# Performance work log

Measured on AMD Instinct MI355X. Metric: run time of the kernel, lower is better.

Reference implementation:

```python
import jax, jax.numpy as jnp
import numpy as np

N_NODES = 100000


def _gcn_conv(h, src, dst, W, b, n_nodes):
    """PyG GCNConv with add_self_loops=True, symmetric normalization.
    out = D^-1/2 (A + I) D^-1/2 (h W) + b, aggregating src->dst."""
    h = h @ W  # transform first (out_dim <= in_dim), as PyG does
    ones = jnp.ones(src.shape[0], dtype=h.dtype)
    deg = jax.ops.segment_sum(ones, dst, num_segments=n_nodes) + 1.0  # +1 self loop
    dinv = jax.lax.rsqrt(deg)
    coef = dinv[src] * dinv[dst]  # per-edge norm
    agg = jax.ops.segment_sum(h[src] * coef[:, None], dst, num_segments=n_nodes)
    agg = agg + h * (dinv * dinv)[:, None]  # self-loop term: dinv_i^2 * h_i
    return agg + b


def setup_inputs() -> dict:
    key = jax.random.key(0)
    k1, k2, k3, k4 = jax.random.split(key, 4)
    x = jax.random.normal(k1, (N_NODES, 256), dtype=jnp.float32)
    edge_index = jax.random.randint(k2, (2, 1600000), 0, N_NODES, dtype=jnp.int64)
    W1 = jax.random.normal(k3, (256, 128), dtype=jnp.float32) * (1.0 / np.sqrt(256))
    b1 = jnp.zeros((128,), dtype=jnp.float32)
    W2 = jax.random.normal(k4, (128, 64), dtype=jnp.float32) * (1.0 / np.sqrt(128))
    b2 = jnp.zeros((64,), dtype=jnp.float32)
    return {"x": x, "edge_index": edge_index, "W1": W1, "b1": b1, "W2": W2, "b2": b2}


def reference(x, edge_index, W1, b1, W2, b2):
    src, dst = edge_index[0], edge_index[1]
    h = jax.nn.relu(_gcn_conv(x, src, dst, W1, b1, N_NODES))
    # dropout is identity in eval mode
    h = _gcn_conv(h, src, dst, W2, b2, N_NODES)
    return jax.nn.log_softmax(h, axis=1)
```

## Files before the change

### kernel.cpp

```cpp
#include <hip/hip_runtime.h>
#include <hip/hip_bf16.h>


#define N_NODES 100000
#define F_IN 256
#define F_MID 128
#define F_OUT 64

#define BSHIFT 8
#define BNODES 256
#define NBUCKETS ((N_NODES + BNODES - 1) / BNODES)
#define BCAP 6144
#define EPB 4096

typedef __attribute__((ext_vector_type(8))) short short8;
typedef __attribute__((ext_vector_type(4))) float f32x4;

__device__ inline ushort bf16_rne(float f) {
    uint u = __float_as_uint(f);
    u += 0x7FFF + ((u >> 16) & 1);
    return (ushort)(u >> 16);
}
__device__ inline float lo16(uint r) { return __uint_as_float(r << 16); }
__device__ inline float hi16(uint r) { return __uint_as_float(r & 0xffff0000u); }
__device__ inline uint pack_bf2(float a, float b) {
    return (uint)bf16_rne(a) | ((uint)bf16_rne(b) << 16);
}


__global__ __launch_bounds__(256)
void bucket_scatter_kernel(const int* __restrict__ src, const int* __restrict__ dst,
                           int* __restrict__ bcur, uint* __restrict__ ebuf, int E) {
    __shared__ int curL[NBUCKETS];
    int t = threadIdx.x;
    int e0 = blockIdx.x * EPB;
    int e1 = e0 + EPB; if (e1 > E) e1 = E;

    for (int i = t; i < NBUCKETS; i += 256) curL[i] = 0;
    __syncthreads();
    for (int i = e0 + t; i < e1; i += 256) atomicAdd(&curL[dst[i] >> BSHIFT], 1);
    __syncthreads();
    for (int i = t; i < NBUCKETS; i += 256) {
        int h = curL[i];
        curL[i] = h ? atomicAdd(&bcur[i], h) : 0;
    }
    __syncthreads();
    for (int i = e0 + t; i < e1; i += 256) {
        int d = dst[i], s = src[i];
        int b = d >> BSHIFT;
        int pos = atomicAdd(&curL[b], 1);
        if (pos < BCAP) ebuf[(size_t)b * BCAP + pos] = ((uint)(d & (BNODES - 1)) << 17) | (uint)s;
    }
}

__global__ __launch_bounds__(256)
void bucket_sort_kernel(const uint* __restrict__ ebuf, const int* __restrict__ bcur,
                        int* __restrict__ ssrc, int* __restrict__ rs, int* __restrict__ cnt,
                        float* __restrict__ dinv, int n) {
    __shared__ uint eL[BCAP];
    __shared__ int hist[BNODES], ps[BNODES];
    int b = blockIdx.x, t = threadIdx.x;
    int nb = bcur[b];
    if (nb > BCAP) nb = BCAP;
    for (int i = t; i < nb; i += 256) eL[i] = ebuf[(size_t)b * BCAP + i];
    hist[t] = 0;
    __syncthreads();
    for (int i = t; i < nb; i += 256) atomicAdd(&hist[eL[i] >> 17], 1);
    __syncthreads();
    ps[t] = hist[t];
    __syncthreads();
#pragma unroll
    for (int off = 1; off < BNODES; off <<= 1) {
        int v = (t >= off) ? ps[t - off] : 0;
        __syncthreads();
        ps[t] += v;
        __syncthreads();
    }
    int excl = ps[t] - hist[t];
    int node = b * BNODES + t;
    if (node < n) {
        rs[node] = b * BCAP + excl;
        cnt[node] = hist[t];
        dinv[node] = 1.0f / sqrtf((float)hist[t] + 1.0f);
    }
    __syncthreads();
    ps[t] = excl;
    __syncthreads();
    for (int i = t; i < nb; i += 256) {
        uint e = eL[i];
        int d = e >> 17;
        int p = atomicAdd(&ps[d], 1);
        ssrc[(size_t)b * BCAP + p] = (int)(e & 0x1FFFF);
    }
}

__global__ __launch_bounds__(256)
void wprep_kernel(const float* __restrict__ W1, const float* __restrict__ W2,
                  short8* __restrict__ W1f, short8* __restrict__ W2f) {
    int b = blockIdx.x;
    if (b < 16) {
        int f = b * 256 + threadIdx.x;
        int k0 = f >> 9, nt = (f >> 6) & 7, ln = f & 63;
        int kbase = k0 * 32 + (ln >> 4) * 8;
        int n = nt * 16 + (ln & 15);
        short8 fr;
#pragma unroll
        for (int j = 0; j < 8; ++j) fr[j] = (short)bf16_rne(W1[(kbase + j) * F_MID + n]);
        W1f[f] = fr;
    } else {
        int f = (b - 16) * 256 + threadIdx.x;
        int k0 = f >> 8, nt = (f >> 6) & 3, ln = f & 63;
        int kbase = k0 * 32 + (ln >> 4) * 8;
        int n = nt * 16 + (ln & 15);
        short8 fr;
#pragma unroll
        for (int j = 0; j < 8; ++j) fr[j] = (short)bf16_rne(W2[(kbase + j) * F_OUT + n]);
        W2f[f] = fr;
    }
}


__global__ __launch_bounds__(512, 4)
void gemm1_kernel(const float* __restrict__ A, const short8* __restrict__ Wf,
                  const float* __restrict__ dinv, ushort* __restrict__ C,
                  int M) {
    __shared__ short8 BsF[4096];
    int tid = threadIdx.x;
    int lane = tid & 63, w = tid >> 6;
    for (int f = tid; f < 4096; f += 512) BsF[f] = Wf[f];
    __syncthreads();

    const float4 z4 = make_float4(0.f, 0.f, 0.f, 0.f);
    int m0 = blockIdx.x * 128 + w * 16;
    int m = m0 + (lane & 15);
    bool mOk = (m < M);
    const float4* aptr = (const float4*)&A[(size_t)(mOk ? m : 0) * F_IN + (lane >> 4) * 8];

    f32x4 acc[8];
#pragma unroll
    for (int nt = 0; nt < 8; ++nt) acc[nt] = (f32x4){0.f, 0.f, 0.f, 0.f};

    float4 v[16];
#pragma unroll
    for (int i = 0; i < 16; ++i) v[i] = mOk ? aptr[(i >> 1) * 8 + (i & 1)] : z4;
#pragma unroll
    for (int i = 0; i < 16; ++i)
        asm volatile("" : "+v"(v[i].x), "+v"(v[i].y), "+v"(v[i].z), "+v"(v[i].w));

#pragma unroll
    for (int k0 = 0; k0 < 8; ++k0) {
        short8 af;
        af[0] = (short)bf16_rne(v[2 * k0].x);     af[1] = (short)bf16_rne(v[2 * k0].y);
        af[2] = (short)bf16_rne(v[2 * k0].z);     af[3] = (short)bf16_rne(v[2 * k0].w);
        af[4] = (short)bf16_rne(v[2 * k0 + 1].x); af[5] = (short)bf16_rne(v[2 * k0 + 1].y);
        af[6] = (short)bf16_rne(v[2 * k0 + 1].z); af[7] = (short)bf16_rne(v[2 * k0 + 1].w);
#pragma unroll
        for (int nt = 0; nt < 8; ++nt) {
            short8 bfr = BsF[(k0 * 8 + nt) * 64 + lane];
            acc[nt] = __builtin_amdgcn_mfma_f32_16x16x32_bf16(af, bfr, acc[nt], 0, 0, 0);
        }
    }
#pragma unroll
    for (int i = 0; i < 4; ++i) {
        int r = m0 + (lane >> 4) * 4 + i;
        if (r < M) {
            float dv = dinv[r];
#pragma unroll
            for (int nt = 0; nt < 8; ++nt)
                C[(size_t)r * F_MID + nt * 16 + (lane & 15)] = bf16_rne(dv * acc[nt][i]);
        }
    }
}

__global__ __launch_bounds__(512, 4)
void gemm2_kernel(const ushort* __restrict__ A, const short8* __restrict__ Wf,
                  const float* __restrict__ dinv, ushort* __restrict__ C,
                  int M) {
    __shared__ short8 BsF[1024];
    int tid = threadIdx.x;
    int lane = tid & 63, w = tid >> 6;
    for (int f = tid; f < 1024; f += 512) BsF[f] = Wf[f];
    __syncthreads();

    int m0 = blockIdx.x * 128 + w * 16;
    int m = m0 + (lane & 15);
    bool mOk = (m < M);

    f32x4 acc[4];
#pragma unroll
    for (int nt = 0; nt < 4; ++nt) acc[nt] = (f32x4){0.f, 0.f, 0.f, 0.f};

    short8 afr[4];
#pragma unroll
    for (int k0 = 0; k0 < 4; ++k0) {
        short8 af = (short8){0, 0, 0, 0, 0, 0, 0, 0};
        if (mOk) af = *(const short8*)&A[(size_t)m * F_MID + k0 * 32 + (lane >> 4) * 8];
        afr[k0] = af;
    }
#pragma unroll
    for (int k0 = 0; k0 < 4; ++k0)
#pragma unroll
        for (int nt = 0; nt < 4; ++nt) {
            short8 bfr = BsF[(k0 * 4 + nt) * 64 + lane];
            acc[nt] = __builtin_amdgcn_mfma_f32_16x16x32_bf16(afr[k0], bfr, acc[nt], 0, 0, 0);
        }
#pragma unroll
    for (int i = 0; i < 4; ++i) {
        int r = m0 + (lane >> 4) * 4 + i;
        if (r < M) {
            float dv = dinv[r];
#pragma unroll
            for (int nt = 0; nt < 4; ++nt)
                C[(size_t)r * F_OUT + nt * 16 + (lane & 15)] = bf16_rne(dv * acc[nt][i]);
        }
    }
}

__global__ __launch_bounds__(256)
void agg1_kernel(const uint4* __restrict__ h, const int* __restrict__ rs,
                 const int* __restrict__ cnt, const int* __restrict__ ssrc,
                 const float* __restrict__ dinv, const float* __restrict__ bias,
                 uint4* __restrict__ outp, int n) {
    int w = threadIdx.x >> 6, lane = threadIdx.x & 63;
    int node = blockIdx.x * 4 + w;
    if (node >= n) return;
    int q = lane >> 4, c16 = lane & 15;
    int start = rs[node], c = cnt[node];
    float dn = dinv[node];
    float a[8];
#pragma unroll
    for (int i = 0; i < 8; ++i) a[i] = 0.f;

    for (int base = 0; base < c; base += 16) {
        bool p[4];
        int s[4];
        uint4 r[4];
#pragma unroll
        for (int j = 0; j < 4; ++j) {
            int e = base + j * 4 + q;
            p[j] = e < c;
            if (p[j]) s[j] = ssrc[start + e];
        }
#pragma unroll
        for (int j = 0; j < 4; ++j)
            if (p[j]) r[j] = h[(size_t)s[j] * 16 + c16];
#pragma unroll
        for (int j = 0; j < 4; ++j) {
            if (p[j]) {
                a[0] += lo16(r[j].x); a[1] += hi16(r[j].x);
                a[2] += lo16(r[j].y); a[3] += hi16(r[j].y);
                a[4] += lo16(r[j].z); a[5] += hi16(r[j].z);
                a[6] += lo16(r[j].w); a[7] += hi16(r[j].w);
            }
        }
    }
#pragma unroll
    for (int i = 0; i < 8; ++i) {
        a[i] += __shfl_xor(a[i], 16);
        a[i] += __shfl_xor(a[i], 32);
    }
    uint4 sr = h[(size_t)node * 16 + c16];
    const float4* b4 = (const float4*)bias;
    float4 b0 = b4[c16 * 2], b1 = b4[c16 * 2 + 1];
    float o0 = fmaxf(fmaf(dn, a[0] + lo16(sr.x), b0.x), 0.f);
    float o1 = fmaxf(fmaf(dn, a[1] + hi16(sr.x), b0.y), 0.f);
    float o2 = fmaxf(fmaf(dn, a[2] + lo16(sr.y), b0.z), 0.f);
    float o3 = fmaxf(fmaf(dn, a[3] + hi16(sr.y), b0.w), 0.f);
    float o4 = fmaxf(fmaf(dn, a[4] + lo16(sr.z), b1.x), 0.f);
    float o5 = fmaxf(fmaf(dn, a[5] + hi16(sr.z), b1.y), 0.f);
    float o6 = fmaxf(fmaf(dn, a[6] + lo16(sr.w), b1.z), 0.f);
    float o7 = fmaxf(fmaf(dn, a[7] + hi16(sr.w), b1.w), 0.f);
    if (q == 0) {
        uint4 ov;
        ov.x = pack_bf2(o0, o1);
        ov.y = pack_bf2(o2, o3);
        ov.z = pack_bf2(o4, o5);
        ov.w = pack_bf2(o6, o7);
        outp[(size_t)node * 16 + c16] = ov;
    }
}

__global__ __launch_bounds__(256)
void agg2_kernel(const uint2* __restrict__ h, const int* __restrict__ rs,
                 const int* __restrict__ cnt, const int* __restrict__ ssrc,
                 const float* __restrict__ dinv, const float* __restrict__ bias,
                 float4* __restrict__ out4, int n) {
    int w = threadIdx.x >> 6, lane = threadIdx.x & 63;
    int node = blockIdx.x * 4 + w;
    if (node >= n) return;
    int q = lane >> 4, c16 = lane & 15;
    int start = rs[node], c = cnt[node];
    float dn = dinv[node];
    float a[4];
#pragma unroll
    for (int i = 0; i < 4; ++i) a[i] = 0.f;

    for (int base = 0; base < c; base += 16) {
        bool p[4];
        int s[4];
        uint2 r[4];
#pragma unroll
        for (int j = 0; j < 4; ++j) {
            int e = base + j * 4 + q;
            p[j] = e < c;
            if (p[j]) s[j] = ssrc[start + e];
        }
#pragma unroll
        for (int j = 0; j < 4; ++j)
            if (p[j]) r[j] = h[(size_t)s[j] * 16 + c16];
#pragma unroll
        for (int j = 0; j < 4; ++j) {
            if (p[j]) {
                a[0] += lo16(r[j].x); a[1] += hi16(r[j].x);
                a[2] += lo16(r[j].y); a[3] += hi16(r[j].y);
            }
        }
    }
#pragma unroll
    for (int i = 0; i < 4; ++i) {
        a[i] += __shfl_xor(a[i], 16);
        a[i] += __shfl_xor(a[i], 32);
    }
    uint2 sr = h[(size_t)node * 16 + c16];
    float4 bv = ((const float4*)bias)[c16];
    float v0 = fmaf(dn, a[0] + lo16(sr.x), bv.x);
    float v1 = fmaf(dn, a[1] + hi16(sr.x), bv.y);
    float v2 = fmaf(dn, a[2] + lo16(sr.y), bv.z);
    float v3 = fmaf(dn, a[3] + hi16(sr.y), bv.w);
    float m = fmaxf(fmaxf(v0, v1), fmaxf(v2, v3));
#pragma unroll
    for (int off = 1; off < 16; off <<= 1) m = fmaxf(m, __shfl_xor(m, off));
    float ssum = expf(v0 - m) + expf(v1 - m) + expf(v2 - m) + expf(v3 - m);
#pragma unroll
    for (int off = 1; off < 16; off <<= 1) ssum += __shfl_xor(ssum, off);
    float lg = m + logf(ssum);
    if (q == 0) out4[(size_t)node * 16 + c16] = make_float4(v0 - lg, v1 - lg, v2 - lg, v3 - lg);
}


extern "C" void kernel_launch(void* const* d_in, const int* in_sizes, int n_in,
                              void* d_out, int out_size, void* d_ws, size_t ws_size,
                              hipStream_t stream) {
    const float* x  = (const float*)d_in[0];
    const int*   ei = (const int*)d_in[1];
    const float* W1 = (const float*)d_in[2];
    const float* b1 = (const float*)d_in[3];
    const float* W2 = (const float*)d_in[4];
    const float* b2 = (const float*)d_in[5];
    float* out = (float*)d_out;

    const int N = N_NODES;
    const int E = in_sizes[1] / 2;
    const int* src = ei;
    const int* dst = ei + E;

    char* ws = (char*)d_ws;
    size_t off = 0;
    auto alloc = [&](size_t bytes) {
        char* p = ws + off;
        off = (off + bytes + 255) & ~(size_t)255;
        return p;
    };
    int*    bcur   = (int*)alloc(NBUCKETS * 4);
    int*    rs     = (int*)alloc(N * 4);
    int*    cnt    = (int*)alloc(N * 4);
    float*  dinv   = (float*)alloc(N * 4);
    short8* W1f    = (short8*)alloc(4096 * 16);
    short8* W2f    = (short8*)alloc(1024 * 16);
    uint*   ebuf   = (uint*)alloc((size_t)NBUCKETS * BCAP * 4);
    int*    ssrc   = (int*)alloc((size_t)NBUCKETS * BCAP * 4);
    uint*   h1     = (uint*)alloc((size_t)N * 64 * 4);
    uint*   h1a    = (uint*)alloc((size_t)N * 64 * 4);
    ushort* h2     = (ushort*)h1;

    const int nScatBlocks = (E + EPB - 1) / EPB;
    const int nAggBlocks  = (N + 3) / 4;
    const int nTiles      = (N + 127) / 128;

    hipMemsetAsync(bcur, 0, NBUCKETS * 4, stream);
    wprep_kernel<<<20, 256, 0, stream>>>(W1, W2, W1f, W2f);

    bucket_scatter_kernel<<<nScatBlocks, 256, 0, stream>>>(src, dst, bcur, ebuf, E);
    bucket_sort_kernel<<<NBUCKETS, 256, 0, stream>>>(ebuf, bcur, ssrc, rs, cnt, dinv, N);

    gemm1_kernel<<<nTiles, 512, 0, stream>>>(x, W1f, dinv, (ushort*)h1, N);
    agg1_kernel<<<nAggBlocks, 256, 0, stream>>>((const uint4*)h1, rs, cnt, ssrc, dinv, b1,
                                                (uint4*)h1a, N);
    gemm2_kernel<<<nTiles, 512, 0, stream>>>((const ushort*)h1a, W2f, dinv, h2, N);
    agg2_kernel<<<nAggBlocks, 256, 0, stream>>>((const uint2*)h2, rs, cnt, ssrc, dinv, b2,
                                                (float4*)out, N);
}
```

Baseline: 391.6 us.

## Stage GEMM1 A tiles through double-buffered swizzled LDS with coalesced loads

GEMM1 now loads the fp32 A tile cooperatively in 64-column chunks with coalesced row-contiguous reads. It converts them to bf16 and stores them in a double-buffered, XOR-swizzled LDS buffer, prefetching the next chunk while MFMAs consume the current one. This replaces the old scheme where each lane held its entire 256-wide row fragment in registers. The aim is better coalescing and lower register pressure. In exchange it adds 32 KB of LDS per block, four block-wide barriers, and a lower launch_bounds occupancy target.

```diff
diff --git a/kernel.cpp b/kernel.cpp
--- a/kernel.cpp
+++ b/kernel.cpp
@@ -120,49 +120,96 @@
 }
 
 
-__global__ __launch_bounds__(512, 4)
+__global__ __launch_bounds__(512, 2)
 void gemm1_kernel(const float* __restrict__ A, const short8* __restrict__ Wf,
                   const float* __restrict__ dinv, ushort* __restrict__ C,
                   int M) {
     __shared__ short8 BsF[4096];
+    __shared__ ushort Abuf[2][128 * 64];
     int tid = threadIdx.x;
     int lane = tid & 63, w = tid >> 6;
+    int m0 = blockIdx.x * 128;
+
+    int o0 = tid * 2;
+    int srow = o0 >> 3;
+    int gr = m0 + srow; if (gr >= M) gr = m0;
+    int cl0 = o0 & 7, cl1 = cl0 + 1;
+    int cg0 = cl0 ^ (srow & 7), cg1 = cl1 ^ (srow & 7);
+    const float* arow = &A[(size_t)gr * F_IN];
+
+    float4 rv[2][2];
+    rv[0][0] = ((const float4*)(arow + cg0 * 8))[0];
+    rv[0][1] = ((const float4*)(arow + cg0 * 8))[1];
+    rv[1][0] = ((const float4*)(arow + cg1 * 8))[0];
+    rv[1][1] = ((const float4*)(arow + cg1 * 8))[1];
+
     for (int f = tid; f < 4096; f += 512) BsF[f] = Wf[f];
-    __syncthreads();
-
-    const float4 z4 = make_float4(0.f, 0.f, 0.f, 0.f);
-    int m0 = blockIdx.x * 128 + w * 16;
-    int m = m0 + (lane & 15);
-    bool mOk = (m < M);
-    const float4* aptr = (const float4*)&A[(size_t)(mOk ? m : 0) * F_IN + (lane >> 4) * 8];
+
+    {
+        short8 pk;
+        pk[0] = (short)bf16_rne(rv[0][0].x); pk[1] = (short)bf16_rne(rv[0][0].y);
+        pk[2] = (short)bf16_rne(rv[0][0].z); pk[3] = (short)bf16_rne(rv[0][0].w);
+        pk[4] = (short)bf16_rne(rv[0][1].x); pk[5] = (short)bf16_rne(rv[0][1].y);
+        pk[6] = (short)bf16_rne(rv[0][1].z); pk[7] = (short)bf16_rne(rv[0][1].w);
+        *(short8*)&Abuf[0][o0 * 8] = pk;
+        pk[0] = (short)bf16_rne(rv[1][0].x); pk[1] = (short)bf16_rne(rv[1][0].y);
+        pk[2] = (short)bf16_rne(rv[1][0].z); pk[3] = (short)bf16_rne(rv[1][0].w);
+        pk[4] = (short)bf16_rne(rv[1][1].x); pk[5] = (short)bf16_rne(rv[1][1].y);
+        pk[6] = (short)bf16_rne(rv[1][1].z); pk[7] = (short)bf16_rne(rv[1][1].w);
+        *(short8*)&Abuf[0][(o0 + 1) * 8] = pk;
+    }
+    __syncthreads();
 
     f32x4 acc[8];
 #pragma unroll
     for (int nt = 0; nt < 8; ++nt) acc[nt] = (f32x4){0.f, 0.f, 0.f, 0.f};
 
-    float4 v[16];
-#pragma unroll
-    for (int i = 0; i < 16; ++i) v[i] = mOk ? aptr[(i >> 1) * 8 + (i & 1)] : z4;
-#pragma unroll
-    for (int i = 0; i < 16; ++i)
-        asm volatile("" : "+v"(v[i].x), "+v"(v[i].y), "+v"(v[i].z), "+v"(v[i].w));
-
-#pragma unroll
-    for (int k0 = 0; k0 < 8; ++k0) {
-        short8 af;
-        af[0] = (short)bf16_rne(v[2 * k0].x);     af[1] = (short)bf16_rne(v[2 * k0].y);
-        af[2] = (short)bf16_rne(v[2 * k0].z);     af[3] = (short)bf16_rne(v[2 * k0].w);
-        af[4] = (short)bf16_rne(v[2 * k0 + 1].x); af[5] = (short)bf16_rne(v[2 * k0 + 1].y);
-        af[6] = (short)bf16_rne(v[2 * k0 + 1].z); af[7] = (short)bf16_rne(v[2 * k0 + 1].w);
-#pragma unroll
-        for (int nt = 0; nt < 8; ++nt) {
-            short8 bfr = BsF[(k0 * 8 + nt) * 64 + lane];
-            acc[nt] = __builtin_amdgcn_mfma_f32_16x16x32_bf16(af, bfr, acc[nt], 0, 0, 0);
-        }
-    }
+    int arow16 = w * 16 + (lane & 15);
+    int asw = arow16 & 7;
+    int abase = arow16 * 8;
+
+#pragma unroll
+    for (int kc = 0; kc < 4; ++kc) {
+        int b = kc & 1;
+        if (kc < 3) {
+            const float* s0 = arow + (kc + 1) * 64 + cg0 * 8;
+            const float* s1 = arow + (kc + 1) * 64 + cg1 * 8;
+            rv[0][0] = ((const float4*)s0)[0];
+            rv[0][1] = ((const float4*)s0)[1];
+            rv[1][0] = ((const float4*)s1)[0];
+            rv[1][1] = ((const float4*)s1)[1];
+            asm volatile("" ::: "memory");
+        }
+#pragma unroll
+        for (int kk = 0; kk < 2; ++kk) {
+            int k0 = kc * 2 + kk;
+            int c = kk * 4 + (lane >> 4);
+            short8 af = *(const short8*)&Abuf[b][(abase + (c ^ asw)) * 8];
+#pragma unroll
+            for (int nt = 0; nt < 8; ++nt) {
+                short8 bfr = BsF[(k0 * 8 + nt) * 64 + lane];
+                acc[nt] = __builtin_amdgcn_mfma_f32_16x16x32_bf16(af, bfr, acc[nt], 0, 0, 0);
+            }
+        }
+        if (kc < 3) {
+            short8 pk;
+            pk[0] = (short)bf16_rne(rv[0][0].x); pk[1] = (short)bf16_rne(rv[0][0].y);
+            pk[2] = (short)bf16_rne(rv[0][0].z); pk[3] = (short)bf16_rne(rv[0][0].w);
+            pk[4] = (short)bf16_rne(rv[0][1].x); pk[5] = (short)bf16_rne(rv[0][1].y);
+            pk[6] = (short)bf16_rne(rv[0][1].z); pk[7] = (short)bf16_rne(rv[0][1].w);
+            *(short8*)&Abuf[b ^ 1][o0 * 8] = pk;
+            pk[0] = (short)bf16_rne(rv[1][0].x); pk[1] = (short)bf16_rne(rv[1][0].y);
+            pk[2] = (short)bf16_rne(rv[1][0].z); pk[3] = (short)bf16_rne(rv[1][0].w);
+            pk[4] = (short)bf16_rne(rv[1][1].x); pk[5] = (short)bf16_rne(rv[1][1].y);
+            pk[6] = (short)bf16_rne(rv[1][1].z); pk[7] = (short)bf16_rne(rv[1][1].w);
+            *(short8*)&Abuf[b ^ 1][(o0 + 1) * 8] = pk;
+        }
+        __syncthreads();
+    }
+
 #pragma unroll
     for (int i = 0; i < 4; ++i) {
-        int r = m0 + (lane >> 4) * 4 + i;
+        int r = blockIdx.x * 128 + w * 16 + (lane >> 4) * 4 + i;
         if (r < M) {
             float dv = dinv[r];
 #pragma unroll
```

Result: faster. 374.1 us (-4.4%).
